# Kernel optimization log

Measured on AMD Instinct MI355X. Metric: run time of the kernel, lower is better.

The kernel has to match this reference:

```python
import jax, jax.numpy as jnp
import numpy as np

H = 16        # num_attention_heads
HS = 128      # head_size
ROT = 32      # rotary_ndims (partial RoPE, NeoX rotary_pct=0.25)
BASE = 10000.0


def _rope_cache(seq_len):
    inv_freq = 1.0 / (BASE ** (jnp.arange(0, ROT, 2, dtype=jnp.float32) / ROT))
    t = jnp.arange(seq_len, dtype=jnp.float32)
    freqs = jnp.outer(t, inv_freq)                      # [s, ROT/2]
    emb = jnp.concatenate([freqs, freqs], axis=-1)      # [s, ROT]
    return jnp.cos(emb), jnp.sin(emb)


def _rotate_half(x):
    x1, x2 = jnp.split(x, 2, axis=-1)
    return jnp.concatenate([-x2, x1], axis=-1)


def setup_inputs() -> dict:
    key = jax.random.key(0)
    k1, k2, k3 = jax.random.split(key, 3)
    B, S, D = 2, 2048, 2048
    hidden_states = jax.random.normal(k1, (B, S, D), dtype=jnp.float32)
    position_ids = jnp.broadcast_to(jnp.arange(S, dtype=jnp.int64 if jax.config.jax_enable_x64 else jnp.int32), (B, S))
    W_qkv = jax.random.normal(k2, (D, 3 * H * HS), dtype=jnp.float32) * 0.02
    b_qkv = jnp.zeros((3 * H * HS,), dtype=jnp.float32)
    W_dense = jax.random.normal(k3, (H * HS, D), dtype=jnp.float32) * 0.02
    b_dense = jnp.zeros((D,), dtype=jnp.float32)
    return {"hidden_states": hidden_states, "position_ids": position_ids,
            "W_qkv": W_qkv, "b_qkv": b_qkv, "W_dense": W_dense, "b_dense": b_dense}


def reference(hidden_states, position_ids, W_qkv, b_qkv, W_dense, b_dense):
    B, S, D = hidden_states.shape
    # fused QKV projection, NeoX layout: [b, s, h, 3*hs]
    qkv = (hidden_states @ W_qkv + b_qkv).reshape(B, S, H, 3 * HS)
    q = qkv[..., :HS]            # [b, s, h, hs]
    k = qkv[..., HS:2 * HS]
    v = qkv[..., 2 * HS:]

    # partial rotary embedding on first ROT dims
    cos, sin = _rope_cache(S)                       # [s, ROT]
    cos = cos[position_ids][:, :, None, :]          # [b, s, 1, ROT]
    sin = sin[position_ids][:, :, None, :]
    q_rot, q_pass = q[..., :ROT], q[..., ROT:]
    k_rot, k_pass = k[..., :ROT], k[..., ROT:]
    q_rot = q_rot * cos + _rotate_half(q_rot) * sin
    k_rot = k_rot * cos + _rotate_half(k_rot) * sin
    q = jnp.concatenate([q_rot, q_pass], axis=-1)
    k = jnp.concatenate([k_rot, k_pass], axis=-1)

    # scaled dot-product attention (no mask, as in the source SDPA call)
    scale = 1.0 / jnp.sqrt(jnp.asarray(HS, dtype=q.dtype))
    scores = jnp.einsum('bqhd,bkhd->bhqk', q, k) * scale   # [b, h, s, s]
    attn = jax.nn.softmax(scores, axis=-1)
    out = jnp.einsum('bhqk,bkhd->bqhd', attn, v)            # [b, s, h, hs]
    out = out.reshape(B, S, H * HS)                         # 'b h d n -> b d (h n)'
    return out @ W_dense + b_dense
```

## Files before the change

### kernel.cpp

```cpp
#include <hip/hip_runtime.h>

typedef short bf16x8 __attribute__((ext_vector_type(8)));
typedef float f32x4 __attribute__((ext_vector_type(4)));

#define S_LEN 2048
#define NHEAD 16
#define HSZ 128

__device__ __forceinline__ float bf2f(ushort u) {
    union { unsigned int i; float f; } x; x.i = ((unsigned int)u) << 16; return x.f;
}
__device__ __forceinline__ ushort f2bf(float f) {
    union { float f; unsigned int i; } x; x.f = f;
    unsigned int r = (x.i + 0x7FFFu + ((x.i >> 16) & 1u)) >> 16;
    return (ushort)r;
}

__device__ __forceinline__ void gload16(const ushort* g, ushort* l) {
    __builtin_amdgcn_global_load_lds(
        (const __attribute__((address_space(1))) unsigned int*)g,
        (__attribute__((address_space(3))) unsigned int*)l,
        16, 0, 0);
}

#define BAR()   asm volatile("s_barrier" ::: "memory")
#define LGKM0() asm volatile("s_waitcnt lgkmcnt(0)" ::: "memory")

__device__ __forceinline__ void transpose_body(
    const float* __restrict__ W, ushort* __restrict__ WT,
    int K, int N, int bx, int by, float (*tile)[33]) {
    int tx = threadIdx.x & 31, ty = threadIdx.x >> 5;
    int n = bx * 32 + tx;
    #pragma unroll
    for (int j = 0; j < 32; j += 8) {
        int k = by * 32 + ty + j;
        tile[ty + j][tx] = W[(size_t)k * N + n];
    }
    __syncthreads();
    int k2 = by * 32 + tx;
    #pragma unroll
    for (int j = 0; j < 32; j += 8) {
        int n2 = bx * 32 + ty + j;
        WT[(size_t)n2 * K + k2] = f2bf(tile[tx][ty + j]);
    }
}

__global__ __launch_bounds__(256) void prep_kernel(
    const float* __restrict__ hidden, ushort* __restrict__ hA,
    const float* __restrict__ Wqkv, ushort* __restrict__ WqT,
    const float* __restrict__ Wd, ushort* __restrict__ WdT) {
    __shared__ float tile[32][33];
    int bid = blockIdx.x;
    if (bid < 8192) {
        int i = bid * 256 + threadIdx.x;
        float4 v = ((const float4*)hidden)[i];
        ushort4 r;
        r.x = f2bf(v.x); r.y = f2bf(v.y); r.z = f2bf(v.z); r.w = f2bf(v.w);
        ((ushort4*)hA)[i] = r;
    } else if (bid < 8192 + 12288) {
        int tb = bid - 8192;
        transpose_body(Wqkv, WqT, 2048, 6144, tb % 192, tb / 192, tile);
    } else {
        int tb = bid - 20480;
        transpose_body(Wd, WdT, 2048, 2048, tb % 64, tb / 64, tile);
    }
}

template <int EPI>
__global__ __launch_bounds__(512, 2) void gemm256(
    const ushort* __restrict__ A, const ushort* __restrict__ Bt,
    const float* __restrict__ bias, float* __restrict__ Cout, int Kdim, int Ndim,
    ushort* __restrict__ q_out, ushort* __restrict__ k_out, ushort* __restrict__ v_out,
    const int* __restrict__ pos_ids) {
    __shared__ __align__(16) ushort lds[65536];
    const int tid = threadIdx.x;
    const int m0 = blockIdx.y * 256, n0 = blockIdx.x * 256;
    const int lane = tid & 63, wid = tid >> 6;
    const int wm = wid >> 2, wn = wid & 3;
    const int lm = lane & 15, quad = lane >> 4;
    const int cs = (quad ^ ((lm >> 1) & 3)) * 8;
    const int aOff = wm * 8192 + lm * 32 + cs;
    const int bOff = 16384 + (wn >> 1) * 8192 + (wn & 1) * 2048 + lm * 32 + cs;
    const int srow = tid >> 2;
    const int xs8 = ((tid & 3) ^ ((tid >> 3) & 3)) * 8;
    const ushort* pAs = A  + (size_t)(m0 + srow) * Kdim + xs8;
    const ushort* pBs = Bt + (size_t)(n0 + srow) * Kdim + xs8;
    const size_t hK = (size_t)128 * Kdim;
    const int sw = wid * 512;

    f32x4 acc[8][4];
    #pragma unroll
    for (int i = 0; i < 8; ++i)
        #pragma unroll
        for (int j = 0; j < 4; ++j) acc[i][j] = (f32x4){0.f, 0.f, 0.f, 0.f};

    const int T = Kdim >> 6;

    auto stageB = [&](int t) {
        ushort* b = lds + (t & 1) * 32768 + 16384 + sw;
        const ushort* g = pBs + (size_t)t * 64;
        gload16(g,            b);
        gload16(g + 32,       b + 4096);
        gload16(g + hK,       b + 8192);
        gload16(g + hK + 32,  b + 12288);
    };
    auto stageA = [&](int t) {
        ushort* b = lds + (t & 1) * 32768 + sw;
        const ushort* g = pAs + (size_t)t * 64;
        gload16(g,            b);
        gload16(g + 32,       b + 4096);
        gload16(g + hK,       b + 8192);
        gload16(g + hK + 32,  b + 12288);
    };

    stageB(0); stageA(0); stageB(1); stageA(1);
    asm volatile("s_waitcnt vmcnt(8)" ::: "memory");
    BAR();

    bf16x8 afC[8], bfC[4], afN[8], bfN[4];
    #pragma unroll
    for (int mt = 0; mt < 8; ++mt) afC[mt] = *(const bf16x8*)(lds + aOff + mt * 512);
    #pragma unroll
    for (int nt = 0; nt < 4; ++nt) bfC[nt] = *(const bf16x8*)(lds + bOff + nt * 512);

    for (int t = 0; t < T; ++t) {
        const ushort* la = lds + (t & 1) * 32768 + aOff;
        const ushort* lb = lds + (t & 1) * 32768 + bOff;
        const bool pf = (t + 2 < T);

        #pragma unroll
        for (int mt = 0; mt < 8; ++mt) afN[mt] = *(const bf16x8*)(la + 4096 + mt * 512);
        #pragma unroll
        for (int nt = 0; nt < 4; ++nt) bfN[nt] = *(const bf16x8*)(lb + 4096 + nt * 512);
        __builtin_amdgcn_s_setprio(1);
        #pragma unroll
        for (int mt = 0; mt < 8; ++mt)
            #pragma unroll
            for (int nt = 0; nt < 4; ++nt)
                acc[mt][nt] = __builtin_amdgcn_mfma_f32_16x16x32_bf16(
                    afC[mt], bfC[nt], acc[mt][nt], 0, 0, 0);
        __builtin_amdgcn_s_setprio(0);
        LGKM0();
        BAR();

        if (pf) { stageB(t + 2); stageA(t + 2); }
        __builtin_amdgcn_s_setprio(1);
        #pragma unroll
        for (int mt = 0; mt < 8; ++mt)
            #pragma unroll
            for (int nt = 0; nt < 4; ++nt)
                acc[mt][nt] = __builtin_amdgcn_mfma_f32_16x16x32_bf16(
                    afN[mt], bfN[nt], acc[mt][nt], 0, 0, 0);
        __builtin_amdgcn_s_setprio(0);
        if (pf) asm volatile("s_waitcnt vmcnt(8)" ::: "memory");
        else    asm volatile("s_waitcnt vmcnt(0)" ::: "memory");
        BAR();

        if (t + 1 < T) {
            const ushort* la2 = lds + ((t + 1) & 1) * 32768 + aOff;
            const ushort* lb2 = lds + ((t + 1) & 1) * 32768 + bOff;
            #pragma unroll
            for (int mt = 0; mt < 8; ++mt) afC[mt] = *(const bf16x8*)(la2 + mt * 512);
            #pragma unroll
            for (int nt = 0; nt < 4; ++nt) bfC[nt] = *(const bf16x8*)(lb2 + nt * 512);
        }
    }

    if (EPI == 0) {
        const int woff = (n0 + wn * 64) % 384;
        const int rot = (woff == 0 || woff == 128) ? 1 : 0;
        float invf = 0.f;
        if (rot) invf = exp2f(-(float)lm * 0.8304820237218405f);
        const int gnb = n0 + wn * 64 + lm;
        #pragma unroll
        for (int mt = 0; mt < 8; ++mt) {
            f32x4 w[4];
            #pragma unroll
            for (int nt = 0; nt < 4; ++nt) {
                float bv = bias[gnb + nt * 16];
                #pragma unroll
                for (int i = 0; i < 4; ++i) w[nt][i] = acc[mt][nt][i] + bv;
            }
            const int gm0 = m0 + wm * 128 + mt * 16 + quad * 4;
            const int b0 = gm0 >> 11, s0 = gm0 & 2047;
            if (rot) {
                #pragma unroll
                for (int i = 0; i < 4; ++i) {
                    float th = (float)pos_ids[b0 * S_LEN + s0 + i] * invf;
                    float sf, cf;
                    sincosf(th, &sf, &cf);
                    float x1 = w[0][i], x2 = w[1][i];
                    w[0][i] = x1 * cf - x2 * sf;
                    w[1][i] = x2 * cf + x1 * sf;
                }
            }
            #pragma unroll
            for (int nt = 0; nt < 4; ++nt) {
                int gn = gnb + nt * 16;
                int h = gn / 384, r = gn - h * 384;
                int tt = r >> 7, d = r & 127;
                if (tt == 2) {
                    ushort4 u;
                    u.x = f2bf(w[nt][0]); u.y = f2bf(w[nt][1]);
                    u.z = f2bf(w[nt][2]); u.w = f2bf(w[nt][3]);
                    *(ushort4*)(v_out + ((size_t)(b0 * NHEAD + h) * HSZ + d) * S_LEN + s0) = u;
                } else {
                    ushort* dst = (tt == 0) ? q_out : k_out;
                    #pragma unroll
                    for (int i = 0; i < 4; ++i)
                        dst[((size_t)(b0 * NHEAD + h) * S_LEN + s0 + i) * HSZ + d] = f2bf(w[nt][i]);
                }
            }
        }
    } else {
        #pragma unroll
        for (int mt = 0; mt < 8; ++mt) {
            #pragma unroll
            for (int nt = 0; nt < 4; ++nt) {
                f32x4 c = acc[mt][nt];
                int gn = n0 + wn * 64 + nt * 16 + lm;
                float bv = bias[gn];
                #pragma unroll
                for (int i = 0; i < 4; ++i) {
                    int gm = m0 + wm * 128 + mt * 16 + quad * 4 + i;
                    Cout[(size_t)gm * Ndim + gn] = c[i] + bv;
                }
            }
        }
    }
}

template <int EPI>
__global__ __launch_bounds__(256) void gemm128(
    const ushort* __restrict__ A, const ushort* __restrict__ Bt,
    const float* __restrict__ bias, float* __restrict__ Cout, int Kdim, int Ndim,
    ushort* __restrict__ q_out, ushort* __restrict__ k_out, ushort* __restrict__ v_out) {
    __shared__ __align__(16) ushort lA[2][128 * 32];
    __shared__ __align__(16) ushort lB[2][128 * 32];
    const int tid = threadIdx.x;
    const int m0 = blockIdx.y * 128, n0 = blockIdx.x * 128;
    const int lane = tid & 63, wid = tid >> 6;
    const int wm = wid >> 1, wn = wid & 1, lm = lane & 15, quad = lane >> 4;
    const int srow = tid >> 2;
    const int gc = (tid & 3) ^ ((tid >> 3) & 3);
    const int wb8 = (wid << 6) * 8;
    const int cs = (quad ^ ((lm >> 1) & 3)) * 8;

    const ushort* pA = A  + (size_t)(m0 + srow) * Kdim + gc * 8;
    const ushort* pB = Bt + (size_t)(n0 + srow) * Kdim + gc * 8;
    const size_t rhalf = (size_t)64 * Kdim;

    const int fA = (wm * 64 + lm) * 32;
    const int fB = (wn * 64 + lm) * 32;

    f32x4 acc[16];
    #pragma unroll
    for (int i = 0; i < 16; ++i) acc[i] = (f32x4){0.f, 0.f, 0.f, 0.f};

    const int T = Kdim >> 5;
    gload16(pA,         lA[0] + wb8);
    gload16(pA + rhalf, lA[0] + 2048 + wb8);
    gload16(pB,         lB[0] + wb8);
    gload16(pB + rhalf, lB[0] + 2048 + wb8);
    pA += 32; pB += 32;

    for (int t = 0; t < T; ++t) {
        __syncthreads();
        const ushort* la = lA[t & 1];
        const ushort* lb = lB[t & 1];
        if (t + 1 < T) {
            ushort* da = lA[(t + 1) & 1];
            ushort* db = lB[(t + 1) & 1];
            gload16(pA,         da + wb8);
            gload16(pA + rhalf, da + 2048 + wb8);
            gload16(pB,         db + wb8);
            gload16(pB + rhalf, db + 2048 + wb8);
            pA += 32; pB += 32;
        }
        bf16x8 af[4], bfr[4];
        #pragma unroll
        for (int t4 = 0; t4 < 4; ++t4) {
            af[t4]  = *(const bf16x8*)(la + fA + t4 * 512 + cs);
            bfr[t4] = *(const bf16x8*)(lb + fB + t4 * 512 + cs);
        }
        #pragma unroll
        for (int mt = 0; mt < 4; ++mt)
            #pragma unroll
            for (int nt = 0; nt < 4; ++nt)
                acc[mt * 4 + nt] = __builtin_amdgcn_mfma_f32_16x16x32_bf16(
                    af[mt], bfr[nt], acc[mt * 4 + nt], 0, 0, 0);
    }

    #pragma unroll
    for (int mt = 0; mt < 4; ++mt) {
        #pragma unroll
        for (int nt = 0; nt < 4; ++nt) {
            f32x4 c = acc[mt * 4 + nt];
            int gn = n0 + wn * 64 + nt * 16 + lm;
            float bv = bias[gn];
            #pragma unroll
            for (int i = 0; i < 4; ++i) {
                int gm = m0 + wm * 64 + mt * 16 + quad * 4 + i;
                float v = c[i] + bv;
                if (EPI == 0) {
                    int h = gn / 384, r = gn - h * 384;
                    int t = r >> 7, d = r & 127;
                    int b = gm >> 11, s = gm & 2047;
                    ushort bb = f2bf(v);
                    if (t == 0) {
                        q_out[((size_t)(b * NHEAD + h) * S_LEN + s) * HSZ + d] = bb;
                    } else if (t == 1) {
                        k_out[((size_t)(b * NHEAD + h) * S_LEN + s) * HSZ + d] = bb;
                    } else {
                        v_out[((size_t)(b * NHEAD + h) * HSZ + d) * S_LEN + s] = bb;
                    }
                } else {
                    Cout[(size_t)gm * Ndim + gn] = v;
                }
            }
        }
    }
}

__global__ __launch_bounds__(512, 2) void attn_mfma(
    const ushort* __restrict__ Q, const ushort* __restrict__ K,
    const ushort* __restrict__ Vt, ushort* __restrict__ O) {
    __shared__ __align__(16) ushort lK[2][128 * 128];
    __shared__ __align__(16) ushort lVt[2][128 * 128];
    __shared__ __align__(16) ushort lP[8 * 32 * 40];

    const int tid = threadIdx.x;
    const int wid = tid >> 6, lane = tid & 63;
    const int L = lane & 15, quad = lane >> 4;
    const int bid0 = blockIdx.y * 8 + blockIdx.x;
    const int swz = (bid0 & 7) * 32 + (bid0 >> 3);
    const int bh = swz >> 3;
    const int q0 = (swz & 7) * 256;
    const int wq0 = wid * 32;
    const size_t base = (size_t)bh * S_LEN * HSZ;
    const ushort* Qb = Q + base + (size_t)q0 * HSZ;
    const ushort* Kb = K + base;
    const ushort* Vb = Vt + base;
    ushort* lPw = lP + wid * (32 * 40);

    bf16x8 qf[2][4];
    #pragma unroll
    for (int qs = 0; qs < 2; ++qs)
        #pragma unroll
        for (int dc = 0; dc < 4; ++dc)
            qf[qs][dc] = *(const bf16x8*)(Qb + (size_t)(wq0 + qs * 16 + L) * HSZ
                                          + dc * 32 + quad * 8);

    int kx[4];
    #pragma unroll
    for (int dc = 0; dc < 4; ++dc) kx[dc] = ((dc * 4 + quad) ^ (L & 7)) * 8;

    const int sr = tid >> 4;
    const int sg = (tid & 15) ^ (sr & 7);
    const int ub = (tid & 0x1C0) * 8;

    f32x4 acc_o[8][2];
    #pragma unroll
    for (int dt = 0; dt < 8; ++dt)
        #pragma unroll
        for (int qs = 0; qs < 2; ++qs) acc_o[dt][qs] = (f32x4){0.f, 0.f, 0.f, 0.f};
    float lacc[2] = {0.f, 0.f};
    const float scale = 0.08838834764831845f;
    const float SHIFT = 12.0f;

    #pragma unroll
    for (int l = 0; l < 4; ++l) {
        int r = sr + l * 32;
        gload16(Kb + (size_t)r * 128 + sg * 8,  lK[0]  + ub + l * 4096);
        gload16(Vb + (size_t)r * 2048 + sg * 8, lVt[0] + ub + l * 4096);
    }

    for (int kt = 0; kt < S_LEN / 128; ++kt) {
        __syncthreads();
        const int cur = kt & 1;
        const ushort* lKc = lK[cur];
        const ushort* lVc = lVt[cur];
        if (kt + 1 < S_LEN / 128) {
            ushort* dK = lK[cur ^ 1];
            ushort* dV = lVt[cur ^ 1];
            int kb = (kt + 1) * 128;
            #pragma unroll
            for (int l = 0; l < 4; ++l) {
                int r = sr + l * 32;
                gload16(Kb + (size_t)(kb + r) * 128 + sg * 8,      dK + ub + l * 4096);
                gload16(Vb + (size_t)r * 2048 + kb + sg * 8,       dV + ub + l * 4096);
            }
        }

        f32x4 sa[8][2];
        #pragma unroll
        for (int t = 0; t < 8; ++t)
            #pragma unroll
            for (int qs = 0; qs < 2; ++qs) sa[t][qs] = (f32x4){0.f, 0.f, 0.f, 0.f};
        #pragma unroll
        for (int t = 0; t < 8; ++t)
            #pragma unroll
            for (int dc = 0; dc < 4; ++dc) {
                bf16x8 kf = *(const bf16x8*)(lKc + (t * 16 + L) * 128 + kx[dc]);
                sa[t][0] = __builtin_amdgcn_mfma_f32_16x16x32_bf16(kf, qf[0][dc], sa[t][0], 0, 0, 0);
                sa[t][1] = __builtin_amdgcn_mfma_f32_16x16x32_bf16(kf, qf[1][dc], sa[t][1], 0, 0, 0);
            }

        #pragma unroll
        for (int h = 0; h < 4; ++h) {
            #pragma unroll
            for (int t2 = 0; t2 < 2; ++t2) {
                int t = h * 2 + t2;
                #pragma unroll
                for (int qs = 0; qs < 2; ++qs) {
                    #pragma unroll
                    for (int r = 0; r < 4; ++r) {
                        float pv = __expf(fmaf(sa[t][qs][r], scale, -SHIFT));
                        lacc[qs] += pv;
                        sa[t][qs][r] = pv;
                    }
                    ushort4 u;
                    u.x = f2bf(sa[t][qs][0]);
                    u.y = f2bf(sa[t][qs][1]);
                    u.z = f2bf(sa[t][qs][2]);
                    u.w = f2bf(sa[t][qs][3]);
                    *(ushort4*)(lPw + (qs * 16 + L) * 40 + t2 * 16 + quad * 4) = u;
                }
            }
            LGKM0();
            bf16x8 pf0 = *(const bf16x8*)(lPw + L * 40 + quad * 8);
            bf16x8 pf1 = *(const bf16x8*)(lPw + (16 + L) * 40 + quad * 8);
            const int vx = ((h * 4 + quad) ^ (L & 7)) * 8;
            #pragma unroll
            for (int dt = 0; dt < 8; ++dt) {
                bf16x8 vf = *(const bf16x8*)(lVc + (dt * 16 + L) * 128 + vx);
                acc_o[dt][0] = __builtin_amdgcn_mfma_f32_16x16x32_bf16(vf, pf0, acc_o[dt][0], 0, 0, 0);
                acc_o[dt][1] = __builtin_amdgcn_mfma_f32_16x16x32_bf16(vf, pf1, acc_o[dt][1], 0, 0, 0);
            }
        }
    }

    const int b = bh >> 4, h = bh & 15;
    #pragma unroll
    for (int qs = 0; qs < 2; ++qs) {
        float l = lacc[qs];
        l += __shfl_xor(l, 16);
        l += __shfl_xor(l, 32);
        float inv = 1.f / l;
        size_t row = ((size_t)(b * S_LEN + q0 + wq0 + qs * 16 + L)) * (NHEAD * HSZ) + h * HSZ;
        #pragma unroll
        for (int dt = 0; dt < 8; ++dt) {
            ushort4 u;
            u.x = f2bf(acc_o[dt][qs][0] * inv);
            u.y = f2bf(acc_o[dt][qs][1] * inv);
            u.z = f2bf(acc_o[dt][qs][2] * inv);
            u.w = f2bf(acc_o[dt][qs][3] * inv);
            *(ushort4*)(O + row + dt * 16 + quad * 4) = u;
        }
    }
}

extern "C" void kernel_launch(void* const* d_in, const int* in_sizes, int n_in,
                              void* d_out, int out_size, void* d_ws, size_t ws_size,
                              hipStream_t stream) {
    const float* hidden = (const float*)d_in[0];
    const int*   pos    = (const int*)d_in[1];
    const float* Wqkv   = (const float*)d_in[2];
    const float* bqkv   = (const float*)d_in[3];
    const float* Wd     = (const float*)d_in[4];
    const float* bd     = (const float*)d_in[5];

    char* ws = (char*)d_ws;
    ushort* hA  = (ushort*)ws;
    ushort* WqT = (ushort*)(ws + 16777216ull);
    ushort* WdT = (ushort*)(ws + 41943040ull);
    ushort* Qb  = (ushort*)(ws + 50331648ull);
    ushort* Kb  = (ushort*)(ws + 67108864ull);
    ushort* Vb  = (ushort*)(ws + 83886080ull);

    prep_kernel<<<dim3(24576), dim3(256), 0, stream>>>(hidden, hA, Wqkv, WqT, Wd, WdT);

    gemm256<0><<<dim3(24, 16), dim3(512), 0, stream>>>(hA, WqT, bqkv, nullptr, 2048, 6144,
                                                       Qb, Kb, Vb, pos);

    ushort* Obuf = hA;
    attn_mfma<<<dim3(8, 32), dim3(512), 0, stream>>>(Qb, Kb, Vb, Obuf);

    gemm128<1><<<dim3(16, 32), dim3(256), 0, stream>>>(Obuf, WdT, bd, (float*)d_out,
                                                       2048, 2048, nullptr, nullptr, nullptr);
}
```

Measured before the change: 406.9 us.

## Retile QKV GEMM to 128x384 blocks aligned with one head

```diff
diff --git a/kernel.cpp b/kernel.cpp
--- a/kernel.cpp
+++ b/kernel.cpp
@@ -66,77 +66,79 @@
     }
 }
 
-template <int EPI>
-__global__ __launch_bounds__(512, 2) void gemm256(
+__global__ __launch_bounds__(512, 2) void gemm_qkv(
     const ushort* __restrict__ A, const ushort* __restrict__ Bt,
-    const float* __restrict__ bias, float* __restrict__ Cout, int Kdim, int Ndim,
+    const float* __restrict__ bias, int Kdim,
     ushort* __restrict__ q_out, ushort* __restrict__ k_out, ushort* __restrict__ v_out,
     const int* __restrict__ pos_ids) {
     __shared__ __align__(16) ushort lds[65536];
     const int tid = threadIdx.x;
-    const int m0 = blockIdx.y * 256, n0 = blockIdx.x * 256;
+    const int m0 = blockIdx.y * 128, n0 = blockIdx.x * 384;
     const int lane = tid & 63, wid = tid >> 6;
     const int wm = wid >> 2, wn = wid & 3;
     const int lm = lane & 15, quad = lane >> 4;
     const int cs = (quad ^ ((lm >> 1) & 3)) * 8;
-    const int aOff = wm * 8192 + lm * 32 + cs;
-    const int bOff = 16384 + (wn >> 1) * 8192 + (wn & 1) * 2048 + lm * 32 + cs;
+    const int aOff = (wm * 64 + lm) * 32 + cs;
+    int bOffs[6];
+    #pragma unroll
+    for (int nt = 0; nt < 6; ++nt) {
+        int rb = wn * 96 + nt * 16;
+        bOffs[nt] = 8192 + (rb >> 7) * 8192 + ((rb & 127) + lm) * 32 + cs;
+    }
     const int srow = tid >> 2;
     const int xs8 = ((tid & 3) ^ ((tid >> 3) & 3)) * 8;
     const ushort* pAs = A  + (size_t)(m0 + srow) * Kdim + xs8;
     const ushort* pBs = Bt + (size_t)(n0 + srow) * Kdim + xs8;
-    const size_t hK = (size_t)128 * Kdim;
+    const size_t gK = (size_t)128 * Kdim;
     const int sw = wid * 512;
 
-    f32x4 acc[8][4];
-    #pragma unroll
-    for (int i = 0; i < 8; ++i)
-        #pragma unroll
-        for (int j = 0; j < 4; ++j) acc[i][j] = (f32x4){0.f, 0.f, 0.f, 0.f};
+    f32x4 acc[4][6];
+    #pragma unroll
+    for (int i = 0; i < 4; ++i)
+        #pragma unroll
+        for (int j = 0; j < 6; ++j) acc[i][j] = (f32x4){0.f, 0.f, 0.f, 0.f};
 
     const int T = Kdim >> 6;
 
     auto stageB = [&](int t) {
-        ushort* b = lds + (t & 1) * 32768 + 16384 + sw;
+        ushort* b = lds + (t & 1) * 32768 + 8192 + sw;
         const ushort* g = pBs + (size_t)t * 64;
-        gload16(g,            b);
-        gload16(g + 32,       b + 4096);
-        gload16(g + hK,       b + 8192);
-        gload16(g + hK + 32,  b + 12288);
+        #pragma unroll
+        for (int gr = 0; gr < 3; ++gr) {
+            gload16(g + gr * gK,      b + gr * 8192);
+            gload16(g + gr * gK + 32, b + gr * 8192 + 4096);
+        }
     };
     auto stageA = [&](int t) {
         ushort* b = lds + (t & 1) * 32768 + sw;
         const ushort* g = pAs + (size_t)t * 64;
-        gload16(g,            b);
-        gload16(g + 32,       b + 4096);
-        gload16(g + hK,       b + 8192);
-        gload16(g + hK + 32,  b + 12288);
+        gload16(g,      b);
+        gload16(g + 32, b + 4096);
     };
 
     stageB(0); stageA(0); stageB(1); stageA(1);
     asm volatile("s_waitcnt vmcnt(8)" ::: "memory");
     BAR();
 
-    bf16x8 afC[8], bfC[4], afN[8], bfN[4];
-    #pragma unroll
-    for (int mt = 0; mt < 8; ++mt) afC[mt] = *(const bf16x8*)(lds + aOff + mt * 512);
-    #pragma unroll
-    for (int nt = 0; nt < 4; ++nt) bfC[nt] = *(const bf16x8*)(lds + bOff + nt * 512);
+    bf16x8 afC[4], bfC[6], afN[4], bfN[6];
+    #pragma unroll
+    for (int mt = 0; mt < 4; ++mt) afC[mt] = *(const bf16x8*)(lds + aOff + mt * 512);
+    #pragma unroll
+    for (int nt = 0; nt < 6; ++nt) bfC[nt] = *(const bf16x8*)(lds + bOffs[nt]);
 
     for (int t = 0; t < T; ++t) {
-        const ushort* la = lds + (t & 1) * 32768 + aOff;
-        const ushort* lb = lds + (t & 1) * 32768 + bOff;
+        const ushort* buf = lds + (t & 1) * 32768;
         const bool pf = (t + 2 < T);
 
         #pragma unroll
-        for (int mt = 0; mt < 8; ++mt) afN[mt] = *(const bf16x8*)(la + 4096 + mt * 512);
-        #pragma unroll
-        for (int nt = 0; nt < 4; ++nt) bfN[nt] = *(const bf16x8*)(lb + 4096 + nt * 512);
+        for (int mt = 0; mt < 4; ++mt) afN[mt] = *(const bf16x8*)(buf + aOff + 4096 + mt * 512);
+        #pragma unroll
+        for (int nt = 0; nt < 6; ++nt) bfN[nt] = *(const bf16x8*)(buf + bOffs[nt] + 4096);
         __builtin_amdgcn_s_setprio(1);
         #pragma unroll
-        for (int mt = 0; mt < 8; ++mt)
-            #pragma unroll
-            for (int nt = 0; nt < 4; ++nt)
+        for (int mt = 0; mt < 4; ++mt)
+            #pragma unroll
+            for (int nt = 0; nt < 6; ++nt)
                 acc[mt][nt] = __builtin_amdgcn_mfma_f32_16x16x32_bf16(
                     afC[mt], bfC[nt], acc[mt][nt], 0, 0, 0);
         __builtin_amdgcn_s_setprio(0);
@@ -146,9 +148,9 @@
         if (pf) { stageB(t + 2); stageA(t + 2); }
         __builtin_amdgcn_s_setprio(1);
         #pragma unroll
-        for (int mt = 0; mt < 8; ++mt)
-            #pragma unroll
-            for (int nt = 0; nt < 4; ++nt)
+        for (int mt = 0; mt < 4; ++mt)
+            #pragma unroll
+            for (int nt = 0; nt < 6; ++nt)
                 acc[mt][nt] = __builtin_amdgcn_mfma_f32_16x16x32_bf16(
                     afN[mt], bfN[nt], acc[mt][nt], 0, 0, 0);
         __builtin_amdgcn_s_setprio(0);
@@ -157,84 +159,63 @@
         BAR();
 
         if (t + 1 < T) {
-            const ushort* la2 = lds + ((t + 1) & 1) * 32768 + aOff;
-            const ushort* lb2 = lds + ((t + 1) & 1) * 32768 + bOff;
-            #pragma unroll
-            for (int mt = 0; mt < 8; ++mt) afC[mt] = *(const bf16x8*)(la2 + mt * 512);
-            #pragma unroll
-            for (int nt = 0; nt < 4; ++nt) bfC[nt] = *(const bf16x8*)(lb2 + nt * 512);
-        }
-    }
-
-    if (EPI == 0) {
-        const int woff = (n0 + wn * 64) % 384;
-        const int rot = (woff == 0 || woff == 128) ? 1 : 0;
-        float invf = 0.f;
-        if (rot) invf = exp2f(-(float)lm * 0.8304820237218405f);
-        const int gnb = n0 + wn * 64 + lm;
-        #pragma unroll
-        for (int mt = 0; mt < 8; ++mt) {
-            f32x4 w[4];
-            #pragma unroll
-            for (int nt = 0; nt < 4; ++nt) {
-                float bv = bias[gnb + nt * 16];
+            const ushort* b2 = lds + ((t + 1) & 1) * 32768;
+            #pragma unroll
+            for (int mt = 0; mt < 4; ++mt) afC[mt] = *(const bf16x8*)(b2 + aOff + mt * 512);
+            #pragma unroll
+            for (int nt = 0; nt < 6; ++nt) bfC[nt] = *(const bf16x8*)(b2 + bOffs[nt]);
+        }
+    }
+
+    const int h = n0 / 384;
+    const int rot = (wn == 0 || wn == 1) ? 1 : 0;
+    const int p0 = (wn == 0) ? 0 : 2;
+    float invf = 0.f;
+    if (rot) invf = exp2f(-(float)lm * 0.8304820237218405f);
+    #pragma unroll
+    for (int mt = 0; mt < 4; ++mt) {
+        f32x4 w[6];
+        #pragma unroll
+        for (int nt = 0; nt < 6; ++nt) {
+            float bv = bias[n0 + wn * 96 + nt * 16 + lm];
+            #pragma unroll
+            for (int i = 0; i < 4; ++i) w[nt][i] = acc[mt][nt][i] + bv;
+        }
+        const int gm0 = m0 + wm * 64 + mt * 16 + quad * 4;
+        const int b0 = gm0 >> 11, s0 = gm0 & 2047;
+        if (rot) {
+            #pragma unroll
+            for (int i = 0; i < 4; ++i) {
+                float th = (float)pos_ids[b0 * S_LEN + s0 + i] * invf;
+                float sf, cf;
+                sincosf(th, &sf, &cf);
+                float x1 = w[p0][i], x2 = w[p0 + 1][i];
+                w[p0][i]     = x1 * cf - x2 * sf;
+                w[p0 + 1][i] = x2 * cf + x1 * sf;
+            }
+        }
+        #pragma unroll
+        for (int nt = 0; nt < 6; ++nt) {
+            int r = wn * 96 + nt * 16 + lm;
+            int tt = r >> 7, d = r & 127;
+            if (tt == 2) {
+                ushort4 u;
+                u.x = f2bf(w[nt][0]); u.y = f2bf(w[nt][1]);
+                u.z = f2bf(w[nt][2]); u.w = f2bf(w[nt][3]);
+                *(ushort4*)(v_out + ((size_t)(b0 * NHEAD + h) * HSZ + d) * S_LEN + s0) = u;
+            } else {
+                ushort* dst = (tt == 0) ? q_out : k_out;
                 #pragma unroll
-                for (int i = 0; i < 4; ++i) w[nt][i] = acc[mt][nt][i] + bv;
-            }
-            const int gm0 = m0 + wm * 128 + mt * 16 + quad * 4;
-            const int b0 = gm0 >> 11, s0 = gm0 & 2047;
-            if (rot) {
-                #pragma unroll
-                for (int i = 0; i < 4; ++i) {
-                    float th = (float)pos_ids[b0 * S_LEN + s0 + i] * invf;
-                    float sf, cf;
-                    sincosf(th, &sf, &cf);
-                    float x1 = w[0][i], x2 = w[1][i];
-                    w[0][i] = x1 * cf - x2 * sf;
-                    w[1][i] = x2 * cf + x1 * sf;
-                }
-            }
-            #pragma unroll
-            for (int nt = 0; nt < 4; ++nt) {
-                int gn = gnb + nt * 16;
-                int h = gn / 384, r = gn - h * 384;
-                int tt = r >> 7, d = r & 127;
-                if (tt == 2) {
-                    ushort4 u;
-                    u.x = f2bf(w[nt][0]); u.y = f2bf(w[nt][1]);
-                    u.z = f2bf(w[nt][2]); u.w = f2bf(w[nt][3]);
-                    *(ushort4*)(v_out + ((size_t)(b0 * NHEAD + h) * HSZ + d) * S_LEN + s0) = u;
-                } else {
-                    ushort* dst = (tt == 0) ? q_out : k_out;
-                    #pragma unroll
-                    for (int i = 0; i < 4; ++i)
-                        dst[((size_t)(b0 * NHEAD + h) * S_LEN + s0 + i) * HSZ + d] = f2bf(w[nt][i]);
-                }
-            }
-        }
-    } else {
-        #pragma unroll
-        for (int mt = 0; mt < 8; ++mt) {
-            #pragma unroll
-            for (int nt = 0; nt < 4; ++nt) {
-                f32x4 c = acc[mt][nt];
-                int gn = n0 + wn * 64 + nt * 16 + lm;
-                float bv = bias[gn];
-                #pragma unroll
-                for (int i = 0; i < 4; ++i) {
-                    int gm = m0 + wm * 128 + mt * 16 + quad * 4 + i;
-                    Cout[(size_t)gm * Ndim + gn] = c[i] + bv;
-                }
-            }
-        }
-    }
-}
-
-template <int EPI>
+                for (int i = 0; i < 4; ++i)
+                    dst[((size_t)(b0 * NHEAD + h) * S_LEN + s0 + i) * HSZ + d] = f2bf(w[nt][i]);
+            }
+        }
+    }
+}
+
 __global__ __launch_bounds__(256) void gemm128(
     const ushort* __restrict__ A, const ushort* __restrict__ Bt,
-    const float* __restrict__ bias, float* __restrict__ Cout, int Kdim, int Ndim,
-    ushort* __restrict__ q_out, ushort* __restrict__ k_out, ushort* __restrict__ v_out) {
+    const float* __restrict__ bias, float* __restrict__ Cout, int Kdim, int Ndim) {
     __shared__ __align__(16) ushort lA[2][128 * 32];
     __shared__ __align__(16) ushort lB[2][128 * 32];
     const int tid = threadIdx.x;
@@ -301,22 +282,7 @@
             #pragma unroll
             for (int i = 0; i < 4; ++i) {
                 int gm = m0 + wm * 64 + mt * 16 + quad * 4 + i;
-                float v = c[i] + bv;
-                if (EPI == 0) {
-                    int h = gn / 384, r = gn - h * 384;
-                    int t = r >> 7, d = r & 127;
-                    int b = gm >> 11, s = gm & 2047;
-                    ushort bb = f2bf(v);
-                    if (t == 0) {
-                        q_out[((size_t)(b * NHEAD + h) * S_LEN + s) * HSZ + d] = bb;
-                    } else if (t == 1) {
-                        k_out[((size_t)(b * NHEAD + h) * S_LEN + s) * HSZ + d] = bb;
-                    } else {
-                        v_out[((size_t)(b * NHEAD + h) * HSZ + d) * S_LEN + s] = bb;
-                    }
-                } else {
-                    Cout[(size_t)gm * Ndim + gn] = v;
-                }
+                Cout[(size_t)gm * Ndim + gn] = c[i] + bv;
             }
         }
     }
@@ -480,12 +446,12 @@
 
     prep_kernel<<<dim3(24576), dim3(256), 0, stream>>>(hidden, hA, Wqkv, WqT, Wd, WdT);
 
-    gemm256<0><<<dim3(24, 16), dim3(512), 0, stream>>>(hA, WqT, bqkv, nullptr, 2048, 6144,
-                                                       Qb, Kb, Vb, pos);
+    gemm_qkv<<<dim3(16, 32), dim3(512), 0, stream>>>(hA, WqT, bqkv, 2048,
+                                                     Qb, Kb, Vb, pos);
 
     ushort* Obuf = hA;
     attn_mfma<<<dim3(8, 32), dim3(512), 0, stream>>>(Qb, Kb, Vb, Obuf);
 
-    gemm128<1><<<dim3(16, 32), dim3(256), 0, stream>>>(Obuf, WdT, bd, (float*)d_out,
-                                                       2048, 2048, nullptr, nullptr, nullptr);
-}
+    gemm128<<<dim3(16, 32), dim3(256), 0, stream>>>(Obuf, WdT, bd, (float*)d_out,
+                                                    2048, 2048);
+}
```

Measured after the change: 447.1 us. +9.9%, slower.
